# Performance work log

Hardware: AMD Instinct MI355X
Metric: run time of the kernel (lower is better)

The kernel has to match this reference:

```python
import jax, jax.numpy as jnp
import numpy as np

D_MODEL = 1024
D_DICT = 16 * D_MODEL  # 16384
K = 32
N_TOKENS = 8192


def setup_inputs() -> dict:
    key = jax.random.key(0)
    k1, k2, k3, k4, k5 = jax.random.split(key, 5)
    x = jax.random.normal(k1, (N_TOKENS, D_MODEL), dtype=jnp.float32)
    # nn.Linear stores weight as [out, in]; y = x @ W.T + b
    W_enc = jax.random.normal(k2, (D_DICT, D_MODEL), dtype=jnp.float32) * 0.02
    b_enc = jax.random.normal(k3, (D_DICT,), dtype=jnp.float32) * 0.02
    W_dec = jax.random.normal(k4, (D_MODEL, D_DICT), dtype=jnp.float32) * 0.02
    b_dec = jax.random.normal(k5, (D_MODEL,), dtype=jnp.float32) * 0.02
    return {"x": x, "W_enc": W_enc, "b_enc": b_enc, "W_dec": W_dec, "b_dec": b_dec}


def reference(x, W_enc, b_enc, W_dec, b_dec):
    # encode: dense linear  [N, d_model] -> [N, d_dict]
    z = x @ W_enc.T + b_enc
    # abs-topk mask along last dim (k < d_dict)
    _, idx = jax.lax.top_k(jnp.abs(z), K)          # idx: [N, K]
    rows = jnp.arange(z.shape[0])[:, None]          # [N, 1]
    mask = jnp.zeros_like(z).at[rows, idx].set(1.0)
    z = z * mask
    # decode: dense linear over full d_dict (mostly zeros)
    recon = z @ W_dec.T + b_dec
    return (recon, z)
```

## Files before the change

### kernel.cpp

```cpp
#include <hip/hip_runtime.h>
#include <stdint.h>

#define M_TOK   8192
#define DMODEL  1024
#define DDICT   16384
#define TOPK    32
#define MAXC    256
#define DELTA   0.03f

typedef __attribute__((ext_vector_type(8))) short bf16x8;
typedef __attribute__((ext_vector_type(4))) float f32x4;

__device__ __forceinline__ unsigned short f32_to_bf16(float f) {
  unsigned u = __float_as_uint(f);
  unsigned r = 0x7FFFu + ((u >> 16) & 1u);
  return (unsigned short)((u + r) >> 16);
}

__device__ __forceinline__ float bf2f(unsigned short h) {
  return __uint_as_float(((unsigned)h) << 16);
}

#define GLD16(g, l)                                                        \
  __builtin_amdgcn_global_load_lds(                                        \
      (const __attribute__((address_space(1))) void*)(g),                  \
      (__attribute__((address_space(3))) void*)(l), 16, 0, 0)

__global__ __launch_bounds__(256) void cast_x_norm_kernel(
    const float* __restrict__ x, unsigned short* __restrict__ xbf,
    float* __restrict__ tau) {
  const int row = blockIdx.x, tid = threadIdx.x;
  const int lane = tid & 63, wave = tid >> 6;
  __shared__ float red[4];
  float4 v = ((const float4*)(x + (size_t)row * DMODEL))[tid];
  ushort4 o;
  o.x = f32_to_bf16(v.x); o.y = f32_to_bf16(v.y);
  o.z = f32_to_bf16(v.z); o.w = f32_to_bf16(v.w);
  ((ushort4*)(xbf + (size_t)row * DMODEL))[tid] = o;
  float ss = v.x * v.x + v.y * v.y + v.z * v.z + v.w * v.w;
#pragma unroll
  for (int off = 32; off; off >>= 1) ss += __shfl_down(ss, off);
  if (lane == 0) red[wave] = ss;
  __syncthreads();
  if (tid == 0) tau[row] = 0.055f * sqrtf(red[0] + red[1] + red[2] + red[3]);
}

__global__ __launch_bounds__(256) void cast_bf16_kernel(
    const float* __restrict__ in, unsigned short* __restrict__ out, int n4) {
  int i = blockIdx.x * 256 + threadIdx.x;
  if (i >= n4) return;
  float4 v = ((const float4*)in)[i];
  ushort4 o;
  o.x = f32_to_bf16(v.x); o.y = f32_to_bf16(v.y);
  o.z = f32_to_bf16(v.z); o.w = f32_to_bf16(v.w);
  ((ushort4*)out)[i] = o;
}

__global__ __launch_bounds__(256) void transpose_bf16_kernel(
    const float* __restrict__ in, unsigned short* __restrict__ out) {
  __shared__ float tile[32][33];
  int tx = threadIdx.x & 31;
  int ty = threadIdx.x >> 5;
  int c0 = blockIdx.x * 32;
  int r0 = blockIdx.y * 32;
#pragma unroll
  for (int i = 0; i < 32; i += 8)
    tile[ty + i][tx] = in[(size_t)(r0 + ty + i) * DDICT + c0 + tx];
  __syncthreads();
#pragma unroll
  for (int i = 0; i < 32; i += 8)
    out[(size_t)(c0 + ty + i) * DMODEL + r0 + tx] = f32_to_bf16(tile[tx][ty + i]);
}

__global__ __launch_bounds__(256, 2) void gemm_enc_kernel(
    const unsigned short* __restrict__ A,
    const unsigned short* __restrict__ B,
    const float* __restrict__ bias,
    const float* __restrict__ tau,
    unsigned* __restrict__ cnt,
    int2* __restrict__ cand,
    float* __restrict__ out_z) {
  __shared__ __align__(16) unsigned short As[2][4][128][8];
  __shared__ float taus[128];

  const int tid  = threadIdx.x;
  const int lane = tid & 63;
  const int wave = tid >> 6;
  const int l16  = lane & 15;
  const int quad = lane >> 4;

  const int lin = blockIdx.x;
  const int xcd = lin & 7;
  const int k   = lin >> 3;
  const int bn  = (xcd + ((k >> 6) << 3)) * 256;
  const int bm  = (k & 63) * 128;
  const int n0 = wave * 64;

  if (tid < 128) taus[tid] = tau[bm + tid];

  const int c0 = tid, c1 = tid + 256;
  const int kc0 = c0 >> 7, r0 = c0 & 127;
  const int kc1 = c1 >> 7, r1 = c1 & 127;
  const unsigned short* Ab = A + (size_t)bm * DMODEL;

  const unsigned short* Bp[4];
#pragma unroll
  for (int j = 0; j < 4; ++j)
    Bp[j] = B + (size_t)(bn + n0 + j * 16 + l16) * DMODEL + quad * 8;

  f32x4 acc[8][4];
#pragma unroll
  for (int i = 0; i < 8; ++i)
#pragma unroll
    for (int j = 0; j < 4; ++j) acc[i][j] = f32x4{0.f, 0.f, 0.f, 0.f};

  bf16x8 b0[4], b1[4];

  GLD16(Ab + (size_t)r0 * DMODEL + kc0 * 8, &As[0][kc0][r0][0]);
  GLD16(Ab + (size_t)r1 * DMODEL + kc1 * 8, &As[0][kc1][r1][0]);
  __builtin_amdgcn_sched_barrier(0);
#pragma unroll
  for (int j = 0; j < 4; ++j) b0[j] = *(const bf16x8*)(Bp[j]);
  __builtin_amdgcn_sched_barrier(0);
  asm volatile("s_waitcnt vmcnt(4)" ::: "memory");
  __builtin_amdgcn_s_barrier();
  __builtin_amdgcn_sched_barrier(0);

#pragma unroll 1
  for (int k0 = 0; k0 < DMODEL; k0 += 64) {
    GLD16(Ab + (size_t)r0 * DMODEL + (k0 + 32) + kc0 * 8, &As[1][kc0][r0][0]);
    GLD16(Ab + (size_t)r1 * DMODEL + (k0 + 32) + kc1 * 8, &As[1][kc1][r1][0]);
    __builtin_amdgcn_sched_barrier(0);
#pragma unroll
    for (int j = 0; j < 4; ++j) b1[j] = *(const bf16x8*)(Bp[j] + k0 + 32);
    __builtin_amdgcn_s_setprio(1);
#pragma unroll
    for (int i = 0; i < 8; ++i) {
      bf16x8 a = *(const bf16x8*)(&As[0][quad][i * 16 + l16][0]);
#pragma unroll
      for (int j = 0; j < 4; ++j)
        acc[i][j] = __builtin_amdgcn_mfma_f32_16x16x32_bf16(a, b0[j], acc[i][j], 0, 0, 0);
    }
    __builtin_amdgcn_s_setprio(0);
    __builtin_amdgcn_sched_barrier(0);
    asm volatile("s_waitcnt vmcnt(4)" ::: "memory");
    __builtin_amdgcn_s_barrier();
    __builtin_amdgcn_sched_barrier(0);

    const bool more = (k0 + 64 < DMODEL);
    if (more) {
      GLD16(Ab + (size_t)r0 * DMODEL + (k0 + 64) + kc0 * 8, &As[0][kc0][r0][0]);
      GLD16(Ab + (size_t)r1 * DMODEL + (k0 + 64) + kc1 * 8, &As[0][kc1][r1][0]);
      __builtin_amdgcn_sched_barrier(0);
#pragma unroll
      for (int j = 0; j < 4; ++j) b0[j] = *(const bf16x8*)(Bp[j] + k0 + 64);
    }
    __builtin_amdgcn_s_setprio(1);
#pragma unroll
    for (int i = 0; i < 8; ++i) {
      bf16x8 a = *(const bf16x8*)(&As[1][quad][i * 16 + l16][0]);
#pragma unroll
      for (int j = 0; j < 4; ++j)
        acc[i][j] = __builtin_amdgcn_mfma_f32_16x16x32_bf16(a, b1[j], acc[i][j], 0, 0, 0);
    }
    __builtin_amdgcn_s_setprio(0);
    if (more) {
      __builtin_amdgcn_sched_barrier(0);
      asm volatile("s_waitcnt vmcnt(4)" ::: "memory");
      __builtin_amdgcn_s_barrier();
      __builtin_amdgcn_sched_barrier(0);
    }
  }

  {
    float* zt = out_z + (size_t)bm * DDICT + bn;
    const float4 z4 = make_float4(0.f, 0.f, 0.f, 0.f);
#pragma unroll
    for (int s = 0; s < 32; ++s) {
      int p = s * 256 + tid;
      int rr = p >> 6, cc = p & 63;
      ((float4*)(zt + (size_t)rr * DDICT))[cc] = z4;
    }
  }

#pragma unroll
  for (int j = 0; j < 4; ++j) {
    int coll = n0 + j * 16 + l16;
    float bv = bias[bn + coll];
#pragma unroll
    for (int i = 0; i < 8; ++i)
#pragma unroll
      for (int r = 0; r < 4; ++r) {
        int rl = i * 16 + quad * 4 + r;
        float z = acc[i][j][r] + bv;
        if (__builtin_fabsf(z) >= taus[rl]) {
          int row = bm + rl;
          unsigned p = atomicAdd(&cnt[row], 1u);
          if (p < MAXC)
            cand[(size_t)row * MAXC + p] = make_int2(bn + coll, __float_as_int(z));
        }
      }
  }
}

__global__ __launch_bounds__(256) void select_kernel(
    const float* __restrict__ x,
    const float* __restrict__ Wenc,
    const float* __restrict__ benc,
    const unsigned short* __restrict__ wdTb,
    const float* __restrict__ bdec,
    const unsigned* __restrict__ cnt,
    const int2* __restrict__ cand,
    float* __restrict__ out_recon,
    float* __restrict__ out_z) {
  const int lane = threadIdx.x & 63;
  const int wave = threadIdx.x >> 6;
  const int row  = blockIdx.x * 4 + wave;

  float4 x4[4];
  const float4* xrow4 = (const float4*)(x + (size_t)row * DMODEL);
#pragma unroll
  for (int t = 0; t < 4; ++t) x4[t] = xrow4[lane + t * 64];

  int n = (int)cnt[row];
  if (n > MAXC) n = MAXC;
  int ccol[4]; float cval[4]; unsigned ckey[4]; bool act[4];
#pragma unroll
  for (int c = 0; c < 4; ++c) {
    const int idx = c * 64 + lane;
    act[c] = idx < n;
    ccol[c] = 0x7FFFFFFF; cval[c] = 0.f; ckey[c] = 0u;
    if (act[c]) {
      int2 cv = cand[(size_t)row * MAXC + idx];
      ccol[c] = cv.x;
      cval[c] = __int_as_float(cv.y);
      ckey[c] = (unsigned)cv.y & 0x7FFFFFFFu;
    }
  }

  const int nw = n < TOPK ? n : TOPK;
  unsigned lo = 0u, hi = 0x7F800000u;
  for (int it = 0; it < 28; ++it) {
    const unsigned mid = (lo + hi) >> 1;
    int tot = 0;
#pragma unroll
    for (int c = 0; c < 4; ++c)
      tot += __popcll(__ballot(act[c] && ckey[c] >= mid));
    if (tot >= nw) lo = mid; else hi = mid;
  }
  const float t32 = __uint_as_float(lo);

  bool fin[4], amb[4];
#pragma unroll
  for (int c = 0; c < 4; ++c) {
    const float ab = __uint_as_float(ckey[c]);
    fin[c] = act[c] && (ab > t32 + DELTA);
    amb[c] = act[c] && !fin[c] && (ab >= t32 - DELTA);
  }
  int nI = 0, nA = 0;
#pragma unroll
  for (int c = 0; c < 4; ++c) {
    nI += __popcll(__ballot(fin[c]));
    nA += __popcll(__ballot(amb[c]));
  }

  double dval[4] = {0.0, 0.0, 0.0, 0.0};
#pragma unroll
  for (int c = 0; c < 4; ++c) {
    unsigned long long bits = __ballot(amb[c]);
    while (bits) {
      const int src = __ffsll(bits) - 1;
      bits &= bits - 1;
      const int j = __shfl(ccol[c], src);
      const float4* wr4 = (const float4*)(Wenc + (size_t)j * DMODEL);
      double s = 0.0;
#pragma unroll
      for (int t = 0; t < 4; ++t) {
        const float4 wv = wr4[lane + t * 64];
        s += (double)x4[t].x * (double)wv.x + (double)x4[t].y * (double)wv.y +
             (double)x4[t].z * (double)wv.z + (double)x4[t].w * (double)wv.w;
      }
#pragma unroll
      for (int off = 32; off; off >>= 1) s += __shfl_down(s, off);
      const double dv = __shfl(s, 0) + (double)benc[j];
      if (lane == src) {
#pragma unroll
        for (int cc = 0; cc < 4; ++cc)
          if (cc == c) dval[cc] = dv;
      }
    }
  }

  int need = TOPK - nI;
  if (need < 0) need = 0;
  if (need > nA) need = nA;
  for (int pick = 0; pick < need; ++pick) {
    double ba = -1.0; int bcol = 0x7FFFFFFF; int bslot = -1;
#pragma unroll
    for (int c = 0; c < 4; ++c)
      if (amb[c]) {
        const double va = fabs(dval[c]);
        if (va > ba || (va == ba && ccol[c] < bcol)) {
          ba = va; bcol = ccol[c]; bslot = c;
        }
      }
    int bl = lane;
#pragma unroll
    for (int off = 32; off; off >>= 1) {
      const double oa = __shfl_down(ba, off);
      const int    oc = __shfl_down(bcol, off);
      const int    ol = __shfl_down(bl, off);
      if (oa > ba || (oa == ba && oc < bcol)) { ba = oa; bcol = oc; bl = ol; }
    }
    bl = __shfl(bl, 0);
    if (lane == bl) {
#pragma unroll
      for (int c = 0; c < 4; ++c)
        if (c == bslot) {
          amb[c] = false;
          fin[c] = true;
          cval[c] = (float)dval[c];
        }
    }
  }

  float ax[16];
  {
    const float4* b4 = (const float4*)bdec;
    float4 t0 = b4[2 * lane],       t1 = b4[2 * lane + 1];
    float4 t2 = b4[128 + 2 * lane], t3 = b4[129 + 2 * lane];
    ax[0] = t0.x; ax[1] = t0.y; ax[2]  = t0.z; ax[3]  = t0.w;
    ax[4] = t1.x; ax[5] = t1.y; ax[6]  = t1.z; ax[7]  = t1.w;
    ax[8] = t2.x; ax[9] = t2.y; ax[10] = t2.z; ax[11] = t2.w;
    ax[12] = t3.x; ax[13] = t3.y; ax[14] = t3.z; ax[15] = t3.w;
  }
#pragma unroll
  for (int c = 0; c < 4; ++c) {
    unsigned long long bits = __ballot(fin[c]);
    while (bits) {
      const int src = __ffsll(bits) - 1;
      bits &= bits - 1;
      const int   j  = __shfl(ccol[c], src);
      const float zv = __shfl(cval[c], src);
      const unsigned short* wrow = wdTb + (size_t)j * DMODEL;
      bf16x8 w0 = ((const bf16x8*)wrow)[lane];
      bf16x8 w1 = ((const bf16x8*)wrow)[lane + 64];
#pragma unroll
      for (int k = 0; k < 8; ++k) {
        ax[k]     = fmaf(zv, bf2f((unsigned short)w0[k]), ax[k]);
        ax[8 + k] = fmaf(zv, bf2f((unsigned short)w1[k]), ax[8 + k]);
      }
    }
  }
  {
    float4* r4 = (float4*)(out_recon + (size_t)row * DMODEL);
    r4[2 * lane]       = make_float4(ax[0], ax[1], ax[2], ax[3]);
    r4[2 * lane + 1]   = make_float4(ax[4], ax[5], ax[6], ax[7]);
    r4[128 + 2 * lane] = make_float4(ax[8], ax[9], ax[10], ax[11]);
    r4[129 + 2 * lane] = make_float4(ax[12], ax[13], ax[14], ax[15]);
  }

  float* zrow = out_z + (size_t)row * DDICT;
#pragma unroll
  for (int c = 0; c < 4; ++c)
    if (fin[c]) zrow[ccol[c]] = cval[c];
}

extern "C" void kernel_launch(void* const* d_in, const int* in_sizes, int n_in,
                              void* d_out, int out_size, void* d_ws, size_t ws_size,
                              hipStream_t stream) {
  const float* x    = (const float*)d_in[0];
  const float* Wenc = (const float*)d_in[1];
  const float* benc = (const float*)d_in[2];
  const float* Wdec = (const float*)d_in[3];
  const float* bdec = (const float*)d_in[4];

  float* out_recon = (float*)d_out;
  float* out_z     = (float*)d_out + (size_t)M_TOK * DMODEL;

  char* w = (char*)d_ws;
  unsigned short* xbf  = (unsigned short*)w;                w += (size_t)M_TOK * DMODEL * 2;
  unsigned short* wbf  = (unsigned short*)w;                w += (size_t)DDICT * DMODEL * 2;
  unsigned short* wdTb = (unsigned short*)w;                w += (size_t)DDICT * DMODEL * 2;
  int2*           cand = (int2*)w;                          w += (size_t)M_TOK * MAXC * 8;
  float*          tau  = (float*)w;                         w += (size_t)M_TOK * 4;
  unsigned*       cnt  = (unsigned*)w;

  hipMemsetAsync(cnt, 0, (size_t)M_TOK * 4, stream);

  cast_x_norm_kernel<<<M_TOK, 256, 0, stream>>>(x, xbf, tau);
  {
    int n4 = DDICT * DMODEL / 4;
    cast_bf16_kernel<<<(n4 + 255) / 256, 256, 0, stream>>>(Wenc, wbf, n4);
  }
  {
    dim3 g(DDICT / 32, DMODEL / 32);
    transpose_bf16_kernel<<<g, 256, 0, stream>>>(Wdec, wdTb);
  }
  {
    gemm_enc_kernel<<<(DDICT / 256) * (M_TOK / 128), 256, 0, stream>>>(
        xbf, wbf, benc, tau, cnt, cand, out_z);
  }
  select_kernel<<<M_TOK / 4, 256, 0, stream>>>(x, Wenc, benc, wdTb, bdec, cnt, cand,
                                               out_recon, out_z);
}
```

Baseline: 1.342 ms.

## Use 256x256 encoder GEMM tiles with LDS-staged B and triple buffering

The encoder GEMM moves from 128x256 tiles (4 waves, B fragments loaded straight from global into registers) to 256x256 tiles with 8 waves in a 2x4 layout. Both A and B are now staged in LDS through global_load_lds, using an XOR swizzle on the k-chunk to avoid bank conflicts. A three-stage buffer keeps two tiles in flight. The aim is higher operand reuse per byte fetched and better latency hiding, at the cost of more LDS per block and possibly lower occupancy.

```diff
diff --git a/kernel.cpp b/kernel.cpp
--- a/kernel.cpp
+++ b/kernel.cpp
@@ -72,7 +72,7 @@
     out[(size_t)(c0 + ty + i) * DMODEL + r0 + tx] = f32_to_bf16(tile[tx][ty + i]);
 }
 
-__global__ __launch_bounds__(256, 2) void gemm_enc_kernel(
+__global__ __launch_bounds__(512, 2) void gemm_enc_kernel(
     const unsigned short* __restrict__ A,
     const unsigned short* __restrict__ B,
     const float* __restrict__ bias,
@@ -80,33 +80,33 @@
     unsigned* __restrict__ cnt,
     int2* __restrict__ cand,
     float* __restrict__ out_z) {
-  __shared__ __align__(16) unsigned short As[2][4][128][8];
-  __shared__ float taus[128];
+  __shared__ __align__(16) unsigned short As[3][256][32];
+  __shared__ __align__(16) unsigned short Bs[3][256][32];
+  __shared__ float taus[256];
 
   const int tid  = threadIdx.x;
   const int lane = tid & 63;
   const int wave = tid >> 6;
   const int l16  = lane & 15;
   const int quad = lane >> 4;
+  const int wm   = (wave >> 2) * 128;
+  const int wn   = (wave & 3) * 64;
 
   const int lin = blockIdx.x;
   const int xcd = lin & 7;
   const int k   = lin >> 3;
-  const int bn  = (xcd + ((k >> 6) << 3)) * 256;
-  const int bm  = (k & 63) * 128;
-  const int n0 = wave * 64;
-
-  if (tid < 128) taus[tid] = tau[bm + tid];
-
-  const int c0 = tid, c1 = tid + 256;
-  const int kc0 = c0 >> 7, r0 = c0 & 127;
-  const int kc1 = c1 >> 7, r1 = c1 & 127;
+  const int bn  = (xcd + ((k >> 5) << 3)) * 256;
+  const int bm  = (k & 31) * 256;
+
+  if (tid < 256) taus[tid] = tau[bm + tid];
+
+  const int rq  = tid >> 2;
+  const int kcs = tid & 3;
+  const int colOff = (kcs ^ (rq & 3)) * 8;
   const unsigned short* Ab = A + (size_t)bm * DMODEL;
-
-  const unsigned short* Bp[4];
-#pragma unroll
-  for (int j = 0; j < 4; ++j)
-    Bp[j] = B + (size_t)(bn + n0 + j * 16 + l16) * DMODEL + quad * 8;
+  const unsigned short* Bb = B + (size_t)bn * DMODEL;
+
+  const int rdk = (quad ^ (l16 & 3)) * 8;
 
   f32x4 acc[8][4];
 #pragma unroll
@@ -114,70 +114,81 @@
 #pragma unroll
     for (int j = 0; j < 4; ++j) acc[i][j] = f32x4{0.f, 0.f, 0.f, 0.f};
 
-  bf16x8 b0[4], b1[4];
-
-  GLD16(Ab + (size_t)r0 * DMODEL + kc0 * 8, &As[0][kc0][r0][0]);
-  GLD16(Ab + (size_t)r1 * DMODEL + kc1 * 8, &As[0][kc1][r1][0]);
-  __builtin_amdgcn_sched_barrier(0);
-#pragma unroll
-  for (int j = 0; j < 4; ++j) b0[j] = *(const bf16x8*)(Bp[j]);
+#define STAGE(sb, kt)                                                         \
+  do {                                                                        \
+    const int kk = (kt) * 32 + colOff;                                        \
+    GLD16(Ab + (size_t)rq * DMODEL + kk,          &As[sb][rq][kcs * 8]);      \
+    GLD16(Ab + (size_t)(rq + 128) * DMODEL + kk,  &As[sb][rq + 128][kcs * 8]);\
+    GLD16(Bb + (size_t)rq * DMODEL + kk,          &Bs[sb][rq][kcs * 8]);      \
+    GLD16(Bb + (size_t)(rq + 128) * DMODEL + kk,  &Bs[sb][rq + 128][kcs * 8]);\
+  } while (0)
+
+#define COMPUTE(cb)                                                           \
+  do {                                                                        \
+    bf16x8 bf[4], af[4];                                                      \
+    _Pragma("unroll")                                                         \
+    for (int j = 0; j < 4; ++j)                                               \
+      bf[j] = *(const bf16x8*)(&Bs[cb][wn + j * 16 + l16][rdk]);              \
+    _Pragma("unroll")                                                         \
+    for (int i = 0; i < 4; ++i)                                               \
+      af[i] = *(const bf16x8*)(&As[cb][wm + i * 16 + l16][rdk]);              \
+    __builtin_amdgcn_s_setprio(1);                                            \
+    _Pragma("unroll")                                                         \
+    for (int i = 0; i < 4; ++i)                                               \
+      _Pragma("unroll")                                                       \
+      for (int j = 0; j < 4; ++j)                                             \
+        acc[i][j] = __builtin_amdgcn_mfma_f32_16x16x32_bf16(af[i], bf[j],     \
+                                                            acc[i][j], 0, 0, 0); \
+    __builtin_amdgcn_s_setprio(0);                                            \
+    __builtin_amdgcn_sched_barrier(0);                                        \
+    _Pragma("unroll")                                                         \
+    for (int i = 0; i < 4; ++i)                                               \
+      af[i] = *(const bf16x8*)(&As[cb][wm + 64 + i * 16 + l16][rdk]);         \
+    __builtin_amdgcn_s_setprio(1);                                            \
+    _Pragma("unroll")                                                         \
+    for (int i = 0; i < 4; ++i)                                               \
+      _Pragma("unroll")                                                       \
+      for (int j = 0; j < 4; ++j)                                             \
+        acc[4 + i][j] = __builtin_amdgcn_mfma_f32_16x16x32_bf16(af[i], bf[j], \
+                                                            acc[4 + i][j], 0, 0, 0); \
+    __builtin_amdgcn_s_setprio(0);                                            \
+  } while (0)
+
+  STAGE(0, 0);
+  STAGE(1, 1);
   __builtin_amdgcn_sched_barrier(0);
   asm volatile("s_waitcnt vmcnt(4)" ::: "memory");
   __builtin_amdgcn_s_barrier();
   __builtin_amdgcn_sched_barrier(0);
 
+  int cb = 0, sb = 2;
 #pragma unroll 1
-  for (int k0 = 0; k0 < DMODEL; k0 += 64) {
-    GLD16(Ab + (size_t)r0 * DMODEL + (k0 + 32) + kc0 * 8, &As[1][kc0][r0][0]);
-    GLD16(Ab + (size_t)r1 * DMODEL + (k0 + 32) + kc1 * 8, &As[1][kc1][r1][0]);
-    __builtin_amdgcn_sched_barrier(0);
-#pragma unroll
-    for (int j = 0; j < 4; ++j) b1[j] = *(const bf16x8*)(Bp[j] + k0 + 32);
-    __builtin_amdgcn_s_setprio(1);
-#pragma unroll
-    for (int i = 0; i < 8; ++i) {
-      bf16x8 a = *(const bf16x8*)(&As[0][quad][i * 16 + l16][0]);
-#pragma unroll
-      for (int j = 0; j < 4; ++j)
-        acc[i][j] = __builtin_amdgcn_mfma_f32_16x16x32_bf16(a, b0[j], acc[i][j], 0, 0, 0);
-    }
-    __builtin_amdgcn_s_setprio(0);
-    __builtin_amdgcn_sched_barrier(0);
-    asm volatile("s_waitcnt vmcnt(4)" ::: "memory");
-    __builtin_amdgcn_s_barrier();
-    __builtin_amdgcn_sched_barrier(0);
-
-    const bool more = (k0 + 64 < DMODEL);
-    if (more) {
-      GLD16(Ab + (size_t)r0 * DMODEL + (k0 + 64) + kc0 * 8, &As[0][kc0][r0][0]);
-      GLD16(Ab + (size_t)r1 * DMODEL + (k0 + 64) + kc1 * 8, &As[0][kc1][r1][0]);
+  for (int kt = 0; kt < 32; ++kt) {
+    if (kt < 30) {
+      STAGE(sb, kt + 2);
       __builtin_amdgcn_sched_barrier(0);
-#pragma unroll
-      for (int j = 0; j < 4; ++j) b0[j] = *(const bf16x8*)(Bp[j] + k0 + 64);
-    }
-    __builtin_amdgcn_s_setprio(1);
-#pragma unroll
-    for (int i = 0; i < 8; ++i) {
-      bf16x8 a = *(const bf16x8*)(&As[1][quad][i * 16 + l16][0]);
-#pragma unroll
-      for (int j = 0; j < 4; ++j)
-        acc[i][j] = __builtin_amdgcn_mfma_f32_16x16x32_bf16(a, b1[j], acc[i][j], 0, 0, 0);
-    }
-    __builtin_amdgcn_s_setprio(0);
-    if (more) {
+    }
+    COMPUTE(cb);
+    if (kt < 31) {
       __builtin_amdgcn_sched_barrier(0);
-      asm volatile("s_waitcnt vmcnt(4)" ::: "memory");
+      if (kt == 30) asm volatile("s_waitcnt vmcnt(0)" ::: "memory");
+      else          asm volatile("s_waitcnt vmcnt(4)" ::: "memory");
       __builtin_amdgcn_s_barrier();
       __builtin_amdgcn_sched_barrier(0);
     }
-  }
+    cb = (cb == 2) ? 0 : cb + 1;
+    sb = (sb == 2) ? 0 : sb + 1;
+  }
+
+#undef COMPUTE
+#undef STAGE
 
   {
     float* zt = out_z + (size_t)bm * DDICT + bn;
     const float4 z4 = make_float4(0.f, 0.f, 0.f, 0.f);
 #pragma unroll
     for (int s = 0; s < 32; ++s) {
-      int p = s * 256 + tid;
+      int p = s * 512 + tid;
       int rr = p >> 6, cc = p & 63;
       ((float4*)(zt + (size_t)rr * DDICT))[cc] = z4;
     }
@@ -185,13 +196,13 @@
 
 #pragma unroll
   for (int j = 0; j < 4; ++j) {
-    int coll = n0 + j * 16 + l16;
+    int coll = wn + j * 16 + l16;
     float bv = bias[bn + coll];
 #pragma unroll
     for (int i = 0; i < 8; ++i)
 #pragma unroll
       for (int r = 0; r < 4; ++r) {
-        int rl = i * 16 + quad * 4 + r;
+        int rl = wm + i * 16 + quad * 4 + r;
         float z = acc[i][j][r] + bv;
         if (__builtin_fabsf(z) >= taus[rl]) {
           int row = bm + rl;
@@ -346,9 +357,9 @@
       bf16x8 w0 = ((const bf16x8*)wrow)[lane];
       bf16x8 w1 = ((const bf16x8*)wrow)[lane + 64];
 #pragma unroll
-      for (int k = 0; k < 8; ++k) {
-        ax[k]     = fmaf(zv, bf2f((unsigned short)w0[k]), ax[k]);
-        ax[8 + k] = fmaf(zv, bf2f((unsigned short)w1[k]), ax[8 + k]);
+      for (int kq = 0; kq < 8; ++kq) {
+        ax[kq]     = fmaf(zv, bf2f((unsigned short)w0[kq]), ax[kq]);
+        ax[8 + kq] = fmaf(zv, bf2f((unsigned short)w1[kq]), ax[8 + kq]);
       }
     }
   }
@@ -398,7 +409,7 @@
     transpose_bf16_kernel<<<g, 256, 0, stream>>>(Wdec, wdTb);
   }
   {
-    gemm_enc_kernel<<<(DDICT / 256) * (M_TOK / 128), 256, 0, stream>>>(
+    gemm_enc_kernel<<<(DDICT / 256) * (M_TOK / 256), 512, 0, stream>>>(
         xbf, wbf, benc, tau, cnt, cand, out_z);
   }
   select_kernel<<<M_TOK / 4, 256, 0, stream>>>(x, Wenc, benc, wdTb, bdec, cnt, cand,
```

After: 1.306 ms. 2.7% less time.
